# Performance work log

Measured on AMD Instinct MI355X. Metric: run time of the kernel, lower is better.

Reference implementation:

```python
import jax, jax.numpy as jnp
import numpy as np
from jax import lax

# Fixed-point format: Q*.8 (8 fractional bits), as used by HGRNFixed8bit's
# to_fixed/from_fixed round-trip. We simulate it in float via round(x*256)/256.
FRAC = 256.0
EPS = 1e-5
B, T, D = 4, 2048, 2048  # batch, seq_len, hidden_size; input_dim = D (expand_ratio=1)


def to_fixed(x):
    return jnp.round(x * FRAC) / FRAC


def to_ternary(w):
    # BitNet-style ternarization: sign(w/mean|w|), zeroed where |w_norm| < 0.5
    scale = jnp.mean(jnp.abs(w))
    wn = w / (scale + 1e-5)
    t = jnp.sign(wn)
    return jnp.where(jnp.abs(wn) < 0.5, 0.0, t).astype(jnp.float32)


def per_channel_scale(w):
    # compute_scale: mean |w| over dim 0, stored in fixed point
    return to_fixed(jnp.mean(jnp.abs(w), axis=0))


def setup_inputs() -> dict:
    key = jax.random.key(0)
    ks = jax.random.split(key, 6)
    hidden_states = jax.random.normal(ks[0], (B, T, D), dtype=jnp.float32)
    # float master weights, then quantize exactly as quantize_weights() does
    w_i_f = jax.random.normal(ks[1], (D, D), dtype=jnp.float32) * 0.02  # i_proj.weight.T
    w_f_f = jax.random.normal(ks[2], (D, D), dtype=jnp.float32) * 0.02  # f_proj.weight.T
    w_g_f = jax.random.normal(ks[3], (D, D), dtype=jnp.float32) * 0.02  # g_proj.weight.T
    w_o_f = jax.random.normal(ks[4], (D, D), dtype=jnp.float32) * 0.02  # o_proj.weight [D_out, D_in]
    g_norm_w = jnp.ones((D,), dtype=jnp.float32)  # g_norm (RMSNorm-swish-gate) weight
    return {
        "hidden_states": hidden_states,
        "w_i": to_ternary(w_i_f), "w_f": to_ternary(w_f_f),
        "w_g": to_ternary(w_g_f), "w_o": to_ternary(w_o_f),
        "s_i": per_channel_scale(w_i_f), "s_f": per_channel_scale(w_f_f),
        "s_g": per_channel_scale(w_g_f), "s_o": per_channel_scale(w_o_f),
        "g_norm_w": g_norm_w,
    }


def reference(hidden_states, w_i, w_f, w_g, w_o, s_i, s_f, s_g, s_o, g_norm_w):
    # Quantize activations to 8-bit fixed point (to_fixed)
    x = to_fixed(hidden_states)                       # [B,T,D]
    # Ternary dequant-matmuls with per-channel scales
    i = jnp.einsum('btd,de->bte', x, w_i) * s_i       # input branch
    f = jax.nn.sigmoid(jnp.einsum('btd,de->bte', x, w_f) * s_f)  # forget gate
    g = jnp.einsum('btd,de->bte', x, w_g) * s_g       # output gate
    i = (1.0 - f) * i                                 # HGRN input gating
    # Gated linear recurrence h_t = f_t * h_{t-1} + i_t via associative scan
    def combine(a, b):
        af, ai = a
        bf, bi = b
        return (af * bf, ai * bf + bi)
    _, h = lax.associative_scan(combine, (f, i), axis=1)  # [B,T,E]
    # FusedRMSNormSwishGate: rmsnorm(h) * weight * swish(g)
    rms = h * lax.rsqrt(jnp.mean(h * h, axis=-1, keepdims=True) + EPS)
    o = rms * g_norm_w * (g * jax.nn.sigmoid(g))
    # Output ternary matmul (o_proj, weight untransposed -> use w_o.T),
    # per-input-channel scale, then from_fixed round-trip of the fixed output
    out = to_fixed(jnp.einsum('bte,oe->bto', o * s_o, w_o))  # [B,T,D]
    return out
```

## Files before the change

kernel.cpp:

```cpp
#include <hip/hip_runtime.h>
#include <hip/hip_bf16.h>
#include <stdint.h>
#include <math.h>


#define BATCH 4
#define SEQ   2048
#define DIM   2048
#define MROWS (BATCH*SEQ)
#define TCH   64
#define NCH   (SEQ/TCH)

#define GBM 256
#define GBN 256
#define GBK 64
#define GNT (DIM/GBK)
#define HALF 8192
#define SLOT (4*HALF)

typedef unsigned short u16;
typedef __attribute__((ext_vector_type(8))) short short8;
typedef __attribute__((ext_vector_type(4))) float f32x4;

static __device__ __forceinline__ u16 f2bf_rne(float x) {
  uint32_t u = __float_as_uint(x);
  u += 0x7FFFu + ((u >> 16) & 1u);
  return (u16)(u >> 16);
}
static __device__ __forceinline__ float bf2f(u16 h) {
  return __uint_as_float(((uint32_t)h) << 16);
}

static __device__ __forceinline__ void gl2lds16(const void* g, void* l) {
  __builtin_amdgcn_global_load_lds((const __attribute__((address_space(1))) void*)g,
                                   (__attribute__((address_space(3))) void*)l,
                                   16, 0, 0);
}

__global__ __launch_bounds__(256) void diag_ws(float* __restrict__ out, float val) {
  size_t i = ((size_t)blockIdx.x * 256 + threadIdx.x) * 8;
#pragma unroll
  for (int j = 0; j < 8; j++) out[i + j] = val;
}

__global__ __launch_bounds__(256) void prep_x(const float* __restrict__ x,
                                              u16* __restrict__ XB) {
  size_t i = ((size_t)blockIdx.x * 256 + threadIdx.x) * 4;
  float4 v = *(const float4*)(x + i);
  float q[4] = {v.x, v.y, v.z, v.w};
  u16 hh[4];
#pragma unroll
  for (int j = 0; j < 4; j++) {
    float xq = rintf(q[j] * 256.0f) * 0.00390625f;
    hh[j] = f2bf_rne(xq);
  }
  *(uint2*)(XB + i) = make_uint2((uint32_t)hh[0] | ((uint32_t)hh[1] << 16),
                                 (uint32_t)hh[2] | ((uint32_t)hh[3] << 16));
}

__global__ void prep_wT(const float* __restrict__ w_i, const float* __restrict__ w_f,
                        const float* __restrict__ w_g, u16* __restrict__ WT) {
  __shared__ u16 tile[32][33];
  const int g = blockIdx.z;
  const float* __restrict__ w = (g == 0) ? w_i : (g == 1) ? w_f : w_g;
  u16* __restrict__ outp = WT + (size_t)g * DIM * DIM;
  const int d0 = blockIdx.x * 32;
  const int e0 = blockIdx.y * 32;
  const int tx = threadIdx.x;
  const int ty = threadIdx.y;
  for (int ii = ty; ii < 32; ii += 8)
    tile[ii][tx] = f2bf_rne(w[(size_t)(d0 + ii) * DIM + e0 + tx]);
  __syncthreads();
  for (int ii = ty; ii < 32; ii += 8)
    outp[(size_t)(e0 + ii) * DIM + d0 + tx] = tile[tx][ii];
}

__global__ __launch_bounds__(256) void prep_wo(const float* __restrict__ w, u16* __restrict__ WB) {
  size_t i = ((size_t)blockIdx.x * 256 + threadIdx.x) * 4;
  float4 v = *(const float4*)(w + i);
  *(uint2*)(WB + i) = make_uint2((uint32_t)f2bf_rne(v.x) | ((uint32_t)f2bf_rne(v.y) << 16),
                                 (uint32_t)f2bf_rne(v.z) | ((uint32_t)f2bf_rne(v.w) << 16));
}

static __device__ __forceinline__ void stage_half(const u16* g, u16* l, int tid) {
  gl2lds16(g, l + (size_t)tid * 8);
  gl2lds16(g + (size_t)64 * DIM, l + (size_t)(tid + 512) * 8);
}

static __device__ __forceinline__ void kloop256(const u16* __restrict__ Ag,
                                                const u16* __restrict__ Bg,
                                                u16* lds, f32x4 (&acc)[8][4]) {
  const int tid = threadIdx.x;
  const int lane16 = tid & 15;
  const int quad = (tid & 63) >> 4;
  const int wid = tid >> 6;
  const int wR = wid >> 2;
  const int wC = wid & 3;

  const int rowS = tid >> 3;
  const int ccS = ((tid & 7) ^ (rowS & 7)) * 8;
  const u16* gA = Ag + (size_t)rowS * DIM + ccS;
  const u16* gB = Bg + (size_t)rowS * DIM + ccS;
  const size_t gH = (size_t)128 * DIM;

  const int cswz = lane16 & 7;
  const int ck0 = (quad ^ cswz) * 8;
  const int ck1 = ((4 + quad) ^ cswz) * 8;
  const int arow = (wR * 64 + lane16) * 64;
  const int brow = (wC * 32 + lane16) * 64;

  stage_half(gA,      lds + 0 * HALF, tid);
  stage_half(gB,      lds + 2 * HALF, tid);
  stage_half(gB + gH, lds + 3 * HALF, tid);
  stage_half(gA + gH, lds + 1 * HALF, tid);
  asm volatile("s_waitcnt vmcnt(4)" ::: "memory");
  __builtin_amdgcn_s_barrier();

  short8 af[4][2], bl[2][2], bh[2][2];

#pragma unroll 1
  for (int t = 0; t < GNT; ++t) {
    const u16* S = lds + (t & 1) * SLOT;
    u16* SN = lds + ((t + 1) & 1) * SLOT;
    const bool pf = (t + 1 < GNT);
    const size_t tg = (size_t)(t + 1) * GBK;

#pragma unroll
    for (int mi = 0; mi < 4; mi++) {
      const u16* aa = S + arow + mi * 1024;
      af[mi][0] = *(const short8*)(aa + ck0);
      af[mi][1] = *(const short8*)(aa + ck1);
    }
#pragma unroll
    for (int ni = 0; ni < 2; ni++) {
      const u16* bb = S + 2 * HALF + brow + ni * 1024;
      bl[ni][0] = *(const short8*)(bb + ck0);
      bl[ni][1] = *(const short8*)(bb + ck1);
    }
    if (pf) stage_half(gA + tg, SN + 0 * HALF, tid);
    __builtin_amdgcn_s_barrier();
    __builtin_amdgcn_s_setprio(1);
#pragma unroll
    for (int mi = 0; mi < 4; mi++)
#pragma unroll
      for (int ni = 0; ni < 2; ni++) {
        acc[mi][ni] = __builtin_amdgcn_mfma_f32_16x16x32_bf16(af[mi][0], bl[ni][0], acc[mi][ni], 0, 0, 0);
        acc[mi][ni] = __builtin_amdgcn_mfma_f32_16x16x32_bf16(af[mi][1], bl[ni][1], acc[mi][ni], 0, 0, 0);
      }
    __builtin_amdgcn_s_setprio(0);
    if (pf) { asm volatile("s_waitcnt vmcnt(4)" ::: "memory"); }
    else    { asm volatile("s_waitcnt vmcnt(2)" ::: "memory"); }
    __builtin_amdgcn_s_barrier();

#pragma unroll
    for (int ni = 0; ni < 2; ni++) {
      const u16* bb = S + 3 * HALF + brow + ni * 1024;
      bh[ni][0] = *(const short8*)(bb + ck0);
      bh[ni][1] = *(const short8*)(bb + ck1);
    }
    if (pf) stage_half(gB + tg, SN + 2 * HALF, tid);
    __builtin_amdgcn_s_barrier();
    __builtin_amdgcn_s_setprio(1);
#pragma unroll
    for (int mi = 0; mi < 4; mi++)
#pragma unroll
      for (int ni = 0; ni < 2; ni++) {
        acc[mi][2 + ni] = __builtin_amdgcn_mfma_f32_16x16x32_bf16(af[mi][0], bh[ni][0], acc[mi][2 + ni], 0, 0, 0);
        acc[mi][2 + ni] = __builtin_amdgcn_mfma_f32_16x16x32_bf16(af[mi][1], bh[ni][1], acc[mi][2 + ni], 0, 0, 0);
      }
    __builtin_amdgcn_s_setprio(0);
    if (pf) { asm volatile("s_waitcnt vmcnt(4)" ::: "memory"); }
    else    { asm volatile("s_waitcnt vmcnt(0)" ::: "memory"); }
    __builtin_amdgcn_s_barrier();

#pragma unroll
    for (int mi = 0; mi < 4; mi++) {
      const u16* aa = S + HALF + arow + mi * 1024;
      af[mi][0] = *(const short8*)(aa + ck0);
      af[mi][1] = *(const short8*)(aa + ck1);
    }
    if (pf) stage_half(gB + gH + tg, SN + 3 * HALF, tid);
    __builtin_amdgcn_s_barrier();
    __builtin_amdgcn_s_setprio(1);
#pragma unroll
    for (int mi = 0; mi < 4; mi++)
#pragma unroll
      for (int ni = 0; ni < 2; ni++) {
        acc[4 + mi][ni] = __builtin_amdgcn_mfma_f32_16x16x32_bf16(af[mi][0], bl[ni][0], acc[4 + mi][ni], 0, 0, 0);
        acc[4 + mi][ni] = __builtin_amdgcn_mfma_f32_16x16x32_bf16(af[mi][1], bl[ni][1], acc[4 + mi][ni], 0, 0, 0);
      }
    __builtin_amdgcn_s_setprio(0);
    __builtin_amdgcn_s_barrier();

    if (pf) stage_half(gA + gH + tg, SN + 1 * HALF, tid);
    __builtin_amdgcn_s_barrier();
    __builtin_amdgcn_s_setprio(1);
#pragma unroll
    for (int mi = 0; mi < 4; mi++)
#pragma unroll
      for (int ni = 0; ni < 2; ni++) {
        acc[4 + mi][2 + ni] = __builtin_amdgcn_mfma_f32_16x16x32_bf16(af[mi][0], bh[ni][0], acc[4 + mi][2 + ni], 0, 0, 0);
        acc[4 + mi][2 + ni] = __builtin_amdgcn_mfma_f32_16x16x32_bf16(af[mi][1], bh[ni][1], acc[4 + mi][2 + ni], 0, 0, 0);
      }
    __builtin_amdgcn_s_setprio(0);
    if (pf) { asm volatile("s_waitcnt vmcnt(4)" ::: "memory"); }
    __builtin_amdgcn_s_barrier();
  }
}

__global__ __launch_bounds__(512, 2) void gemm_gates8(
    const u16* __restrict__ XB, const u16* __restrict__ WT,
    const float* __restrict__ s_i, const float* __restrict__ s_f, const float* __restrict__ s_g,
    const float* __restrict__ gnw, const float* __restrict__ s_o,
    u16* __restrict__ Ib, u16* __restrict__ Fb, u16* __restrict__ Gb) {
  __shared__ __align__(16) u16 lds[2 * SLOT];
  const int bid = blockIdx.x;
  const int i = (bid & 7) * 96 + (bid >> 3);
  const int gate = i >> 8;
  const int r = i & 255;
  const int sr = r >> 5;
  const int s = r & 31;
  const int m0 = (sr * 4 + (s & 3)) * GBM;
  const int n0 = (s >> 2) * GBN;

  const u16* Ag = XB + (size_t)m0 * DIM;
  const u16* Bg = WT + (size_t)gate * DIM * DIM + (size_t)n0 * DIM;

  f32x4 acc[8][4];
#pragma unroll
  for (int a = 0; a < 8; a++)
#pragma unroll
    for (int b = 0; b < 4; b++) acc[a][b] = {0.f, 0.f, 0.f, 0.f};

  kloop256(Ag, Bg, lds, acc);

  __syncthreads();
  const int tid = threadIdx.x;
  const int lane16 = tid & 15;
  const int quad = (tid & 63) >> 4;
  const int wid = tid >> 6;
  const int wR = wid >> 2;
  const int wC = wid & 3;
  const float* __restrict__ sc = (gate == 0) ? s_i : (gate == 1) ? s_f : s_g;
  u16* __restrict__ Out = (gate == 0) ? Ib : (gate == 1) ? Fb : Gb;
  u16* T = lds;
#pragma unroll
  for (int p = 0; p < 2; ++p) {
#pragma unroll
    for (int ni = 0; ni < 2; ++ni) {
      const int tcol = wC * 32 + ni * 16 + lane16;
      const int n = n0 + p * 128 + tcol;
      const float scale = sc[n];
      const float post = (gate == 2) ? gnw[n] * s_o[n] : 0.f;
#pragma unroll
      for (int hA = 0; hA < 2; ++hA)
#pragma unroll
        for (int mi = 0; mi < 4; ++mi) {
          const int lrow = hA * 128 + wR * 64 + mi * 16 + quad * 4;
#pragma unroll
          for (int r2 = 0; r2 < 4; ++r2) {
            float v = acc[hA * 4 + mi][p * 2 + ni][r2] * scale;
            if (gate == 1) v = 1.0f / (1.0f + expf(-v));
            if (gate == 2) v = v / (1.0f + expf(-v)) * post;
            T[(lrow + r2) * 136 + tcol] = f2bf_rne(v);
          }
        }
    }
    __syncthreads();
#pragma unroll
    for (int j = 0; j < 8; j++) {
      const int id = tid + j * 512;
      const int row = id >> 4;
      const int c16 = id & 15;
      uint4 v = *(const uint4*)(T + row * 136 + c16 * 8);
      *(uint4*)(Out + (size_t)(m0 + row) * DIM + n0 + p * 128 + c16 * 8) = v;
    }
    __syncthreads();
  }
}

__global__ __launch_bounds__(512, 2) void gemm_out8(const u16* __restrict__ OS,
                                                    const u16* __restrict__ WOB,
                                                    float* __restrict__ out) {
  __shared__ __align__(16) u16 lds[2 * SLOT];
  const int bid = blockIdx.x;
  const int l = bid >> 3;
  const int m0 = ((bid & 7) * 4 + (l & 3)) * GBM;
  const int n0 = (l >> 2) * GBN;

  const u16* Ag = OS + (size_t)m0 * DIM;
  const u16* Bg = WOB + (size_t)n0 * DIM;

  f32x4 acc[8][4];
#pragma unroll
  for (int a = 0; a < 8; a++)
#pragma unroll
    for (int b = 0; b < 4; b++) acc[a][b] = {0.f, 0.f, 0.f, 0.f};

  kloop256(Ag, Bg, lds, acc);

  const int tid = threadIdx.x;
  const int lane16 = tid & 15;
  const int quad = (tid & 63) >> 4;
  const int wid = tid >> 6;
  const int wR = wid >> 2;
  const int wC = wid & 3;
#pragma unroll
  for (int p = 0; p < 2; ++p)
#pragma unroll
    for (int ni = 0; ni < 2; ++ni) {
      const int n = n0 + p * 128 + wC * 32 + ni * 16 + lane16;
#pragma unroll
      for (int hA = 0; hA < 2; ++hA)
#pragma unroll
        for (int mi = 0; mi < 4; ++mi) {
          const int mrow = m0 + hA * 128 + wR * 64 + mi * 16 + quad * 4;
#pragma unroll
          for (int r2 = 0; r2 < 4; ++r2)
            out[(size_t)(mrow + r2) * DIM + n] =
                rintf(acc[hA * 4 + mi][p * 2 + ni][r2] * 256.0f) * 0.00390625f;
        }
    }
}

__global__ __launch_bounds__(256) void scan_phase1(const u16* __restrict__ Fb,
                                                   const u16* __restrict__ Ib,
                                                   float* __restrict__ Pc,
                                                   float* __restrict__ Sc) {
  const int e0 = (blockIdx.x * 256 + threadIdx.x) * 2;
  const int c = blockIdx.y;
  const int b = blockIdx.z;
  const size_t base = ((size_t)b * SEQ + (size_t)c * TCH) * DIM + e0;
  float P0 = 1.f, S0 = 0.f, P1 = 1.f, S1 = 0.f;
  for (int t = 0; t < TCH; t++) {
    const uint32_t fp = *(const uint32_t*)(Fb + base + (size_t)t * DIM);
    const uint32_t ip = *(const uint32_t*)(Ib + base + (size_t)t * DIM);
    const float f0 = bf2f((u16)fp), f1 = bf2f((u16)(fp >> 16));
    const float i0 = bf2f((u16)ip), i1 = bf2f((u16)(ip >> 16));
    S0 = S0 * f0 + (1.f - f0) * i0;  P0 *= f0;
    S1 = S1 * f1 + (1.f - f1) * i1;  P1 *= f1;
  }
  const size_t ci = ((size_t)b * NCH + c) * DIM + e0;
  *(float2*)(Pc + ci) = make_float2(P0, P1);
  *(float2*)(Sc + ci) = make_float2(S0, S1);
}

__global__ __launch_bounds__(256) void scan_phase2(const u16* __restrict__ Fb,
                                                   const u16* __restrict__ Ib,
                                                   const float* __restrict__ Pc,
                                                   const float* __restrict__ Sc,
                                                   u16* __restrict__ Hb) {
  const int e0 = (blockIdx.x * 256 + threadIdx.x) * 2;
  const int c = blockIdx.y;
  const int b = blockIdx.z;
  float h0 = 0.f, h1 = 0.f;
  for (int cc = 0; cc < c; cc++) {
    const size_t ci = ((size_t)b * NCH + cc) * DIM + e0;
    const float2 p = *(const float2*)(Pc + ci);
    const float2 s = *(const float2*)(Sc + ci);
    h0 = s.x + p.x * h0;
    h1 = s.y + p.y * h1;
  }
  const size_t base = ((size_t)b * SEQ + (size_t)c * TCH) * DIM + e0;
  for (int t = 0; t < TCH; t++) {
    const uint32_t fp = *(const uint32_t*)(Fb + base + (size_t)t * DIM);
    const uint32_t ip = *(const uint32_t*)(Ib + base + (size_t)t * DIM);
    const float f0 = bf2f((u16)fp), f1 = bf2f((u16)(fp >> 16));
    const float i0 = bf2f((u16)ip), i1 = bf2f((u16)(ip >> 16));
    h0 = f0 * h0 + (1.f - f0) * i0;
    h1 = f1 * h1 + (1.f - f1) * i1;
    *(uint32_t*)(Hb + base + (size_t)t * DIM) =
        (uint32_t)f2bf_rne(h0) | ((uint32_t)f2bf_rne(h1) << 16);
  }
}

__global__ __launch_bounds__(256) void rms_gate(const u16* __restrict__ Hb,
                                                const u16* __restrict__ SwGb,
                                                u16* __restrict__ OS) {
  const size_t base = (size_t)blockIdx.x * DIM;
  const int tid = threadIdx.x;
  const int e0 = tid * 8;
  uint4 hp = *(const uint4*)(Hb + base + e0);
  float hv[8];
  hv[0] = bf2f((u16)hp.x); hv[1] = bf2f((u16)(hp.x >> 16));
  hv[2] = bf2f((u16)hp.y); hv[3] = bf2f((u16)(hp.y >> 16));
  hv[4] = bf2f((u16)hp.z); hv[5] = bf2f((u16)(hp.z >> 16));
  hv[6] = bf2f((u16)hp.w); hv[7] = bf2f((u16)(hp.w >> 16));
  float ss = 0.f;
#pragma unroll
  for (int j = 0; j < 8; j++) ss += hv[j] * hv[j];
#pragma unroll
  for (int off = 32; off > 0; off >>= 1) ss += __shfl_down(ss, off, 64);
  __shared__ float red[4];
  if ((tid & 63) == 0) red[tid >> 6] = ss;
  __syncthreads();
  const float tot = red[0] + red[1] + red[2] + red[3];
  const float inv = 1.0f / sqrtf(tot * (1.0f / (float)DIM) + 1e-5f);

  uint4 gp = *(const uint4*)(SwGb + base + e0);
  float gv[8];
  gv[0] = bf2f((u16)gp.x); gv[1] = bf2f((u16)(gp.x >> 16));
  gv[2] = bf2f((u16)gp.y); gv[3] = bf2f((u16)(gp.y >> 16));
  gv[4] = bf2f((u16)gp.z); gv[5] = bf2f((u16)(gp.z >> 16));
  gv[6] = bf2f((u16)gp.w); gv[7] = bf2f((u16)(gp.w >> 16));
  u16 ov[8];
#pragma unroll
  for (int j = 0; j < 8; j++) ov[j] = f2bf_rne(hv[j] * inv * gv[j]);
  uint4 op;
  op.x = (uint32_t)ov[0] | ((uint32_t)ov[1] << 16);
  op.y = (uint32_t)ov[2] | ((uint32_t)ov[3] << 16);
  op.z = (uint32_t)ov[4] | ((uint32_t)ov[5] << 16);
  op.w = (uint32_t)ov[6] | ((uint32_t)ov[7] << 16);
  *(uint4*)(OS + base + e0) = op;
}

extern "C" void kernel_launch(void* const* d_in, const int* in_sizes, int n_in,
                              void* d_out, int out_size, void* d_ws, size_t ws_size,
                              hipStream_t stream) {
  (void)in_sizes; (void)n_in; (void)out_size;
  const float* x   = (const float*)d_in[0];
  const float* w_i = (const float*)d_in[1];
  const float* w_f = (const float*)d_in[2];
  const float* w_g = (const float*)d_in[3];
  const float* w_o = (const float*)d_in[4];
  const float* s_i = (const float*)d_in[5];
  const float* s_f = (const float*)d_in[6];
  const float* s_g = (const float*)d_in[7];
  const float* s_o = (const float*)d_in[8];
  const float* gnw = (const float*)d_in[9];
  float* out = (float*)d_out;

  const size_t MB = 1024 * 1024;
  const size_t NEED = 88 * MB;
  if (ws_size < NEED) {
    diag_ws<<<MROWS * DIM / 2048, 256, 0, stream>>>(out, (float)(ws_size / MB));
    return;
  }

  uint8_t* ws = (uint8_t*)d_ws;
  u16* XB = (u16*)(ws);
  u16* WT = (u16*)(ws + 32 * MB);
  u16* Ib = (u16*)(ws + 56 * MB);
  float* Pc = (float*)(ws + 32 * MB);
  float* Sc = (float*)(ws + 33 * MB);
  u16* WOB = (u16*)(ws + 34 * MB);
  u16* Hb  = XB;
  u16* OS  = Ib;
  u16* Gb = (u16*)d_out;
  u16* Fb = (u16*)((uint8_t*)d_out + 32 * MB);

  prep_x<<<MROWS * DIM / 1024, 256, 0, stream>>>(x, XB);
  prep_wT<<<dim3(DIM / 32, DIM / 32, 3), dim3(32, 8, 1), 0, stream>>>(w_i, w_f, w_g, WT);
  gemm_gates8<<<768, 512, 0, stream>>>(XB, WT, s_i, s_f, s_g, gnw, s_o, Ib, Fb, Gb);
  scan_phase1<<<dim3(DIM / 512, NCH, BATCH), 256, 0, stream>>>(Fb, Ib, Pc, Sc);
  scan_phase2<<<dim3(DIM / 512, NCH, BATCH), 256, 0, stream>>>(Fb, Ib, Pc, Sc, Hb);
  prep_wo<<<DIM * DIM / 1024, 256, 0, stream>>>(w_o, WOB);
  rms_gate<<<MROWS, 256, 0, stream>>>(Hb, Gb, OS);
  gemm_out8<<<256, 512, 0, stream>>>(OS, WOB, out);
}
```

Baseline: 507.4 us.

## Deepen GEMM global-to-LDS prefetch to two tiles ahead

Changes the double-buffered GEMM mainloop so it prefetches K-tile t+2 into the slot just consumed, instead of tile t+1 into the other slot. Both LDS slots are staged in the prologue, and the vmcnt waits are reworked so more loads stay in flight during the MFMA phases. The goal is to hide global memory latency more fully. In exchange it carries more outstanding loads, and the in-place overwrite of slot S relies on the barrier and vmcnt accounting being exactly right.

```diff
diff --git a/kernel.cpp b/kernel.cpp
--- a/kernel.cpp
+++ b/kernel.cpp
@@ -109,21 +109,28 @@
   const int arow = (wR * 64 + lane16) * 64;
   const int brow = (wC * 32 + lane16) * 64;
 
-  stage_half(gA,      lds + 0 * HALF, tid);
-  stage_half(gB,      lds + 2 * HALF, tid);
-  stage_half(gB + gH, lds + 3 * HALF, tid);
-  stage_half(gA + gH, lds + 1 * HALF, tid);
-  asm volatile("s_waitcnt vmcnt(4)" ::: "memory");
+  {
+    u16* s0 = lds;
+    u16* s1 = lds + SLOT;
+    stage_half(gA,            s0 + 0 * HALF, tid);
+    stage_half(gB,            s0 + 2 * HALF, tid);
+    stage_half(gB + gH,       s0 + 3 * HALF, tid);
+    stage_half(gA + gH,       s0 + 1 * HALF, tid);
+    stage_half(gA + GBK,      s1 + 0 * HALF, tid);
+    stage_half(gB + GBK,      s1 + 2 * HALF, tid);
+    stage_half(gB + gH + GBK, s1 + 3 * HALF, tid);
+    stage_half(gA + gH + GBK, s1 + 1 * HALF, tid);
+  }
+  asm volatile("s_waitcnt vmcnt(12)" ::: "memory");
   __builtin_amdgcn_s_barrier();
 
   short8 af[4][2], bl[2][2], bh[2][2];
 
 #pragma unroll 1
   for (int t = 0; t < GNT; ++t) {
-    const u16* S = lds + (t & 1) * SLOT;
-    u16* SN = lds + ((t + 1) & 1) * SLOT;
-    const bool pf = (t + 1 < GNT);
-    const size_t tg = (size_t)(t + 1) * GBK;
+    u16* S = lds + (t & 1) * SLOT;
+    const bool pf = (t + 2 < GNT);
+    const size_t tg = (size_t)(t + 2) * GBK;
 
 #pragma unroll
     for (int mi = 0; mi < 4; mi++) {
@@ -137,7 +144,6 @@
       bl[ni][0] = *(const short8*)(bb + ck0);
       bl[ni][1] = *(const short8*)(bb + ck1);
     }
-    if (pf) stage_half(gA + tg, SN + 0 * HALF, tid);
     __builtin_amdgcn_s_barrier();
     __builtin_amdgcn_s_setprio(1);
 #pragma unroll
@@ -148,8 +154,8 @@
         acc[mi][ni] = __builtin_amdgcn_mfma_f32_16x16x32_bf16(af[mi][1], bl[ni][1], acc[mi][ni], 0, 0, 0);
       }
     __builtin_amdgcn_s_setprio(0);
-    if (pf) { asm volatile("s_waitcnt vmcnt(4)" ::: "memory"); }
-    else    { asm volatile("s_waitcnt vmcnt(2)" ::: "memory"); }
+    if (t + 1 < GNT) { asm volatile("s_waitcnt vmcnt(10)" ::: "memory"); }
+    else             { asm volatile("s_waitcnt vmcnt(2)"  ::: "memory"); }
     __builtin_amdgcn_s_barrier();
 
 #pragma unroll
@@ -158,7 +164,10 @@
       bh[ni][0] = *(const short8*)(bb + ck0);
       bh[ni][1] = *(const short8*)(bb + ck1);
     }
-    if (pf) stage_half(gB + tg, SN + 2 * HALF, tid);
+    if (pf) {
+      stage_half(gA + tg, S + 0 * HALF, tid);
+      stage_half(gB + tg, S + 2 * HALF, tid);
+    }
     __builtin_amdgcn_s_barrier();
     __builtin_amdgcn_s_setprio(1);
 #pragma unroll
@@ -169,8 +178,9 @@
         acc[mi][2 + ni] = __builtin_amdgcn_mfma_f32_16x16x32_bf16(af[mi][1], bh[ni][1], acc[mi][2 + ni], 0, 0, 0);
       }
     __builtin_amdgcn_s_setprio(0);
-    if (pf) { asm volatile("s_waitcnt vmcnt(4)" ::: "memory"); }
-    else    { asm volatile("s_waitcnt vmcnt(0)" ::: "memory"); }
+    if (pf)                { asm volatile("s_waitcnt vmcnt(12)" ::: "memory"); }
+    else if (t + 2 == GNT) { asm volatile("s_waitcnt vmcnt(8)"  ::: "memory"); }
+    else                   { asm volatile("s_waitcnt vmcnt(0)"  ::: "memory"); }
     __builtin_amdgcn_s_barrier();
 
 #pragma unroll
@@ -179,7 +189,7 @@
       af[mi][0] = *(const short8*)(aa + ck0);
       af[mi][1] = *(const short8*)(aa + ck1);
     }
-    if (pf) stage_half(gB + gH + tg, SN + 3 * HALF, tid);
+    if (pf) stage_half(gB + gH + tg, S + 3 * HALF, tid);
     __builtin_amdgcn_s_barrier();
     __builtin_amdgcn_s_setprio(1);
 #pragma unroll
@@ -192,7 +202,7 @@
     __builtin_amdgcn_s_setprio(0);
     __builtin_amdgcn_s_barrier();
 
-    if (pf) stage_half(gA + gH + tg, SN + 1 * HALF, tid);
+    if (pf) stage_half(gA + gH + tg, S + 1 * HALF, tid);
     __builtin_amdgcn_s_barrier();
     __builtin_amdgcn_s_setprio(1);
 #pragma unroll
@@ -203,7 +213,8 @@
         acc[4 + mi][2 + ni] = __builtin_amdgcn_mfma_f32_16x16x32_bf16(af[mi][1], bh[ni][1], acc[4 + mi][2 + ni], 0, 0, 0);
       }
     __builtin_amdgcn_s_setprio(0);
-    if (pf) { asm volatile("s_waitcnt vmcnt(4)" ::: "memory"); }
+    if (pf)                { asm volatile("s_waitcnt vmcnt(12)" ::: "memory"); }
+    else if (t + 2 == GNT) { asm volatile("s_waitcnt vmcnt(4)"  ::: "memory"); }
     __builtin_amdgcn_s_barrier();
   }
 }
```

After: 523.5 us. +3.2%, slower.
